# Kernel optimization log

Hardware: AMD Instinct MI355X
Metric: run time of the kernel (lower is better)

Reference implementation:

```python
import jax, jax.numpy as jnp
import numpy as np
import math

B, T, D, H, L = 8, 1024, 128, 8, 2
DH = D // H            # head dim = 16
F = 2 * D              # ffn hidden = 256 (FFN_EXPANSION=2)
SCALE = math.sqrt(DH)  # sqrt of Q last dim per head


def layernorm(x, g, b):
    m = jnp.mean(x, axis=-1, keepdims=True)
    v = jnp.var(x, axis=-1, keepdims=True)
    return (x - m) * jax.lax.rsqrt(v + 1e-5) * g + b


def setup_inputs() -> dict:
    key = jax.random.key(0)
    ks = jax.random.split(key, 16)
    s = 1.0 / math.sqrt(D)
    r = lambda i, shp: jax.random.normal(ks[i], shp, dtype=jnp.float32) * s
    return {
        "x": jax.random.normal(ks[0], (B, T, D), dtype=jnp.float32),
        "y": jax.random.normal(ks[1], (B, T, D), dtype=jnp.float32),
        # shared qkv projections (no bias), per layer
        "Wq": r(2, (L, D, D)), "Wk": r(3, (L, D, D)), "Wv": r(4, (L, D, D)),
        "Wox": r(5, (L, D, D)), "box": jnp.zeros((L, D), jnp.float32),
        "Woy": r(6, (L, D, D)), "boy": jnp.zeros((L, D), jnp.float32),
        "ln1x_g": jnp.ones((L, D), jnp.float32), "ln1x_b": jnp.zeros((L, D), jnp.float32),
        "ln1y_g": jnp.ones((L, D), jnp.float32), "ln1y_b": jnp.zeros((L, D), jnp.float32),
        "ln2x_g": jnp.ones((L, D), jnp.float32), "ln2x_b": jnp.zeros((L, D), jnp.float32),
        "ln2y_g": jnp.ones((L, D), jnp.float32), "ln2y_b": jnp.zeros((L, D), jnp.float32),
        "fx_w1": r(7, (L, D, F)), "fx_b1": jnp.zeros((L, F), jnp.float32),
        "fx_w2": r(8, (L, F, D)), "fx_b2": jnp.zeros((L, D), jnp.float32),
        "fy_w1": r(9, (L, D, F)), "fy_b1": jnp.zeros((L, F), jnp.float32),
        "fy_w2": r(10, (L, F, D)), "fy_b2": jnp.zeros((L, D), jnp.float32),
    }


def _heads(t):
    # (B,T,D) -> (B,T,H,DH)
    return t.reshape(B, T, H, DH)


def _block(x, y, Wq, Wk, Wv, Wox, box, Woy, boy,
           ln1x_g, ln1x_b, ln1y_g, ln1y_b, ln2x_g, ln2x_b, ln2y_g, ln2y_b,
           fx_w1, fx_b1, fx_w2, fx_b2, fy_w1, fy_b1, fy_w2, fy_b2):
    xn = layernorm(x, ln1x_g, ln1x_b)
    yn = layernorm(y, ln1y_g, ln1y_b)
    # x-branch: Q from y, K/V from x ; y-branch: Q from x, K/V from y
    qx = _heads(yn @ Wq); kx = _heads(xn @ Wk); vx = _heads(xn @ Wv)
    qy = _heads(xn @ Wq); ky = _heads(yn @ Wk); vy = _heads(yn @ Wv)
    ax = jnp.einsum('bthd,bshd->bhts', qx, kx)  # (B,H,T,T)
    ay = jnp.einsum('bthd,bshd->bhts', qy, ky)
    # cat over heads + reshape(B,2,H,T,T) + mean(dim=1) == per-head average
    w = jax.nn.softmax((ax + ay) * (0.5 / SCALE), axis=-1)
    o1 = jnp.einsum('bhts,bshd->bthd', w, vx).reshape(B, T, D) @ Wox + box
    o2 = jnp.einsum('bhts,bshd->bthd', w, vy).reshape(B, T, D) @ Woy + boy
    x = x + o1
    y = y + o2
    xn2 = layernorm(x, ln2x_g, ln2x_b)
    yn2 = layernorm(y, ln2y_g, ln2y_b)
    x = x + jax.nn.gelu(xn2 @ fx_w1 + fx_b1, approximate=False) @ fx_w2 + fx_b2
    y = y + jax.nn.gelu(yn2 @ fy_w1 + fy_b1, approximate=False) @ fy_w2 + fy_b2
    return x, y


def reference(x, y, Wq, Wk, Wv, Wox, box, Woy, boy,
              ln1x_g, ln1x_b, ln1y_g, ln1y_b, ln2x_g, ln2x_b, ln2y_g, ln2y_b,
              fx_w1, fx_b1, fx_w2, fx_b2, fy_w1, fy_b1, fy_w2, fy_b2):
    for i in range(L):
        x, y = _block(x, y, Wq[i], Wk[i], Wv[i], Wox[i], box[i], Woy[i], boy[i],
                      ln1x_g[i], ln1x_b[i], ln1y_g[i], ln1y_b[i],
                      ln2x_g[i], ln2x_b[i], ln2y_g[i], ln2y_b[i],
                      fx_w1[i], fx_b1[i], fx_w2[i], fx_b2[i],
                      fy_w1[i], fy_b1[i], fy_w2[i], fy_b2[i])
    return (x, y)
```

## Files before the change

kernel.cpp:

```cpp
#include <hip/hip_runtime.h>
#include <cstddef>

#define BB   8
#define TT   1024
#define DDIM 128
#define HH   8
#define DHH  16
#define FF   256
#define BT   (BB * TT)

typedef unsigned short u16;
typedef __attribute__((ext_vector_type(8))) short short8;
typedef __attribute__((ext_vector_type(4))) float f32x4;

__device__ __forceinline__ u16 bf(float x) {
  unsigned u = __builtin_bit_cast(unsigned, x);
  u += 0x7fffu + ((u >> 16) & 1u);
  return (u16)(u >> 16);
}
__device__ __forceinline__ u16 bft(float x) {
  return (u16)(__builtin_bit_cast(unsigned, x) >> 16);
}
__device__ __forceinline__ float gelu_f(float x) {
  const float t = x * (0.79788456f + 0.03567740814f * x * x);
  return x / (1.0f + __expf(-2.0f * t));
}

__device__ __forceinline__ void qkv_tail(
    const u16* __restrict__ Wq, const u16* __restrict__ Wk, const u16* __restrict__ Wv,
    u16* __restrict__ q_out, u16* __restrict__ k_out, u16* __restrict__ vT_out,
    int m0, u16 (*As)[136], u16 (*Bs)[136]) {
  const int tid = threadIdx.x;
  const int w = tid >> 6, lane = tid & 63, l15 = lane & 15, quad = lane >> 4;
  const int wr = w & 1, wc = w >> 1;
  const u16* Ws[3] = {Wq, Wk, Wv};
  #pragma unroll
  for (int wi = 0; wi < 3; ++wi) {
    #pragma unroll
    for (int t = tid; t < 2048; t += 256) {
      const int r = t >> 4, g8 = (t & 15) << 3;
      *(short8*)&Bs[r][g8] = *(const short8*)(Ws[wi] + (size_t)r * 128 + g8);
    }
    __syncthreads();
    f32x4 acc[4];
    #pragma unroll
    for (int j = 0; j < 4; ++j) acc[j] = {0.f, 0.f, 0.f, 0.f};
    #pragma unroll
    for (int ks = 0; ks < 4; ++ks) {
      const short8 ar = *(const short8*)&As[wr * 16 + l15][ks * 32 + quad * 8];
      #pragma unroll
      for (int j = 0; j < 4; ++j) {
        const short8 br = *(const short8*)&Bs[wc * 64 + j * 16 + l15][ks * 32 + quad * 8];
        acc[j] = __builtin_amdgcn_mfma_f32_16x16x32_bf16(ar, br, acc[j], 0, 0, 0);
      }
    }
    if (wi == 2) {
      const int m_base = m0 + wr * 16 + quad * 4;
      const int bb_ = m_base >> 10, s = m_base & 1023;
      #pragma unroll
      for (int j = 0; j < 4; ++j) {
        const int n = wc * 64 + j * 16 + l15;
        const int h = n >> 4, c = n & 15;
        ushort4 o;
        o.x = bf(acc[j][0]); o.y = bf(acc[j][1]);
        o.z = bf(acc[j][2]); o.w = bf(acc[j][3]);
        *(ushort4*)(vT_out + (((size_t)(bb_ * 8 + h) * 16 + c) << 10) + s) = o;
      }
    } else {
      u16* out = (wi == 0) ? q_out : k_out;
      #pragma unroll
      for (int j = 0; j < 4; ++j) {
        const int n = wc * 64 + j * 16 + l15;
        #pragma unroll
        for (int reg = 0; reg < 4; ++reg) {
          const int m = m0 + wr * 16 + quad * 4 + reg;
          out[(size_t)m * 128 + n] = bf(acc[j][reg]);
        }
      }
    }
    __syncthreads();
  }
}

struct PrepP { const float* W; u16* Wt; int K; int N; };
struct PrepArgs { PrepP p[18]; };

__global__ __launch_bounds__(256) void prep_k(PrepArgs a) {
  const PrepP pp = a.p[blockIdx.z];
  const int n0 = blockIdx.x * 64, k0 = blockIdx.y * 64;
  if (n0 >= pp.N || k0 >= pp.K) return;
  __shared__ float tile[64][65];
  const int tid = threadIdx.x;
  #pragma unroll
  for (int t = tid; t < 1024; t += 256) {
    const int kk = t >> 4, nn4 = (t & 15) << 2;
    float4 v = *(const float4*)(pp.W + (size_t)(k0 + kk) * pp.N + n0 + nn4);
    tile[nn4 + 0][kk] = v.x; tile[nn4 + 1][kk] = v.y;
    tile[nn4 + 2][kk] = v.z; tile[nn4 + 3][kk] = v.w;
  }
  __syncthreads();
  #pragma unroll
  for (int t = tid; t < 1024; t += 256) {
    const int nn = t >> 4, kk4 = (t & 15) << 2;
    ushort4 o;
    o.x = bf(tile[nn][kk4 + 0]); o.y = bf(tile[nn][kk4 + 1]);
    o.z = bf(tile[nn][kk4 + 2]); o.w = bf(tile[nn][kk4 + 3]);
    *(ushort4*)(pp.Wt + (size_t)(n0 + nn) * pp.K + k0 + kk4) = o;
  }
}

struct LnqkvP { const float* in; const float* g; const float* b;
                const u16* Wq; const u16* Wk; const u16* Wv;
                u16* q_out; u16* k_out; u16* vT_out; };
struct LnqkvArgs { LnqkvP p[2]; };

__global__ __launch_bounds__(256) void lnqkv_k(LnqkvArgs a) {
  const LnqkvP pp = a.p[blockIdx.y];
  const int m0 = blockIdx.x * 32;
  __shared__ __align__(16) u16 As[32][136];
  __shared__ __align__(16) u16 Bs[128][136];
  __shared__ float2 stats[32][2];
  const int tid  = threadIdx.x;
  const int w    = tid >> 6;
  const int lane = tid & 63;
  const int l15  = lane & 15;
  const int quad = lane >> 4;
  const int wr = w & 1, wc = w >> 1;

  float xv[4][4];
  #pragma unroll
  for (int j = 0; j < 4; ++j) {
    const int n = wc * 64 + j * 16 + l15;
    #pragma unroll
    for (int reg = 0; reg < 4; ++reg) {
      const int m = m0 + wr * 16 + quad * 4 + reg;
      xv[j][reg] = pp.in[(size_t)m * 128 + n];
    }
  }
  #pragma unroll
  for (int reg = 0; reg < 4; ++reg) {
    float s = 0.f, q = 0.f;
    #pragma unroll
    for (int j = 0; j < 4; ++j) { const float v = xv[j][reg]; s += v; q += v * v; }
    #pragma unroll
    for (int off = 8; off >= 1; off >>= 1) {
      s += __shfl_xor(s, off, 16);
      q += __shfl_xor(q, off, 16);
    }
    if (l15 == 0) stats[wr * 16 + quad * 4 + reg][wc] = make_float2(s, q);
  }
  __syncthreads();
  #pragma unroll
  for (int reg = 0; reg < 4; ++reg) {
    const int mloc = wr * 16 + quad * 4 + reg;
    const float2 s0 = stats[mloc][0], s1 = stats[mloc][1];
    const float mean = (s0.x + s1.x) * (1.0f / 128.f);
    const float var  = (s0.y + s1.y) * (1.0f / 128.f) - mean * mean;
    const float r    = rsqrtf(var + 1e-5f);
    #pragma unroll
    for (int j = 0; j < 4; ++j) {
      const int n = wc * 64 + j * 16 + l15;
      As[mloc][n] = bf((xv[j][reg] - mean) * r * pp.g[n] + pp.b[n]);
    }
  }
  qkv_tail(pp.Wq, pp.Wk, pp.Wv, pp.q_out, pp.k_out, pp.vT_out, m0, As, Bs);
}

struct WofnP { const u16* A; const u16* WoT; const float* bo; const float* res;
               const float* g2; const float* b2l;
               const u16* W1t; const float* b1;
               const u16* W2t; const float* b2;
               float* outF;
               const float* gn; const float* bn;
               const u16* nWq; const u16* nWk; const u16* nWv;
               u16* q_out; u16* k_out; u16* vT_out; };
struct WofnArgs { WofnP p[2]; int ln; };

__global__ __launch_bounds__(256) void wofn_k(WofnArgs a) {
  const WofnP pp = a.p[blockIdx.y];
  const int m0 = blockIdx.x * 32;
  __shared__ __align__(16) u16 As[32][136];
  __shared__ __align__(16) u16 Bs[128][136];
  __shared__ __align__(16) u16 Hs[32][264];
  __shared__ float2 stats[32][2];
  const int tid  = threadIdx.x;
  const int w    = tid >> 6;
  const int lane = tid & 63;
  const int l15  = lane & 15;
  const int quad = lane >> 4;
  const int wr = w & 1, wc = w >> 1;

  #pragma unroll
  for (int t = tid; t < 512; t += 256) {
    const int r = t >> 4, g8 = (t & 15) << 3;
    *(short8*)&As[r][g8] = *(const short8*)(pp.A + (size_t)(m0 + r) * 128 + g8);
  }
  #pragma unroll
  for (int t = tid; t < 2048; t += 256) {
    const int r = t >> 4, g8 = (t & 15) << 3;
    *(short8*)&Bs[r][g8] = *(const short8*)(pp.WoT + (size_t)r * 128 + g8);
  }
  __syncthreads();
  f32x4 acc[4];
  #pragma unroll
  for (int j = 0; j < 4; ++j) acc[j] = {0.f, 0.f, 0.f, 0.f};
  #pragma unroll
  for (int ks = 0; ks < 4; ++ks) {
    const short8 ar = *(const short8*)&As[wr * 16 + l15][ks * 32 + quad * 8];
    #pragma unroll
    for (int j = 0; j < 4; ++j) {
      const short8 br = *(const short8*)&Bs[wc * 64 + j * 16 + l15][ks * 32 + quad * 8];
      acc[j] = __builtin_amdgcn_mfma_f32_16x16x32_bf16(ar, br, acc[j], 0, 0, 0);
    }
  }

  float xv[4][4];
  #pragma unroll
  for (int j = 0; j < 4; ++j) {
    const int n = wc * 64 + j * 16 + l15;
    const float bias_v = pp.bo[n];
    #pragma unroll
    for (int reg = 0; reg < 4; ++reg) {
      const int m = m0 + wr * 16 + quad * 4 + reg;
      xv[j][reg] = acc[j][reg] + bias_v + pp.res[(size_t)m * 128 + n];
    }
  }

  #pragma unroll
  for (int reg = 0; reg < 4; ++reg) {
    float s = 0.f, q = 0.f;
    #pragma unroll
    for (int j = 0; j < 4; ++j) { const float v = xv[j][reg]; s += v; q += v * v; }
    #pragma unroll
    for (int off = 8; off >= 1; off >>= 1) {
      s += __shfl_xor(s, off, 16);
      q += __shfl_xor(q, off, 16);
    }
    if (l15 == 0) stats[wr * 16 + quad * 4 + reg][wc] = make_float2(s, q);
  }
  __syncthreads();
  #pragma unroll
  for (int reg = 0; reg < 4; ++reg) {
    const int mloc = wr * 16 + quad * 4 + reg;
    const float2 s0 = stats[mloc][0], s1 = stats[mloc][1];
    const float mean = (s0.x + s1.x) * (1.0f / 128.f);
    const float var  = (s0.y + s1.y) * (1.0f / 128.f) - mean * mean;
    const float r    = rsqrtf(var + 1e-5f);
    #pragma unroll
    for (int j = 0; j < 4; ++j) {
      const int n = wc * 64 + j * 16 + l15;
      As[mloc][n] = bf((xv[j][reg] - mean) * r * pp.g2[n] + pp.b2l[n]);
    }
  }
  __syncthreads();

  for (int nh = 0; nh < 2; ++nh) {
    #pragma unroll
    for (int t = tid; t < 2048; t += 256) {
      const int r = t >> 4, g8 = (t & 15) << 3;
      *(short8*)&Bs[r][g8] = *(const short8*)(pp.W1t + (size_t)(nh * 128 + r) * 128 + g8);
    }
    __syncthreads();
    f32x4 a1[4];
    #pragma unroll
    for (int j = 0; j < 4; ++j) a1[j] = {0.f, 0.f, 0.f, 0.f};
    #pragma unroll
    for (int ks = 0; ks < 4; ++ks) {
      const short8 ar = *(const short8*)&As[wr * 16 + l15][ks * 32 + quad * 8];
      #pragma unroll
      for (int j = 0; j < 4; ++j) {
        const short8 br = *(const short8*)&Bs[wc * 64 + j * 16 + l15][ks * 32 + quad * 8];
        a1[j] = __builtin_amdgcn_mfma_f32_16x16x32_bf16(ar, br, a1[j], 0, 0, 0);
      }
    }
    #pragma unroll
    for (int j = 0; j < 4; ++j) {
      const int n = wc * 64 + j * 16 + l15;
      const float bias_v = pp.b1[nh * 128 + n];
      #pragma unroll
      for (int reg = 0; reg < 4; ++reg) {
        const int mloc = wr * 16 + quad * 4 + reg;
        Hs[mloc][nh * 128 + n] = bf(gelu_f(a1[j][reg] + bias_v));
      }
    }
    __syncthreads();
  }

  f32x4 a2[4];
  #pragma unroll
  for (int j = 0; j < 4; ++j) a2[j] = {0.f, 0.f, 0.f, 0.f};
  for (int kh = 0; kh < 2; ++kh) {
    #pragma unroll
    for (int t = tid; t < 2048; t += 256) {
      const int r = t >> 4, g8 = (t & 15) << 3;
      *(short8*)&Bs[r][g8] = *(const short8*)(pp.W2t + (size_t)r * 256 + kh * 128 + g8);
    }
    __syncthreads();
    #pragma unroll
    for (int ks = 0; ks < 4; ++ks) {
      const short8 ar = *(const short8*)&Hs[wr * 16 + l15][kh * 128 + ks * 32 + quad * 8];
      #pragma unroll
      for (int j = 0; j < 4; ++j) {
        const short8 br = *(const short8*)&Bs[wc * 64 + j * 16 + l15][ks * 32 + quad * 8];
        a2[j] = __builtin_amdgcn_mfma_f32_16x16x32_bf16(ar, br, a2[j], 0, 0, 0);
      }
    }
    __syncthreads();
  }

  #pragma unroll
  for (int j = 0; j < 4; ++j) {
    const int n = wc * 64 + j * 16 + l15;
    const float bias_v = pp.b2[n];
    #pragma unroll
    for (int reg = 0; reg < 4; ++reg) {
      const int m = m0 + wr * 16 + quad * 4 + reg;
      const float v = a2[j][reg] + bias_v + xv[j][reg];
      xv[j][reg] = v;
      pp.outF[(size_t)m * 128 + n] = v;
    }
  }
  if (!a.ln) return;

  #pragma unroll
  for (int reg = 0; reg < 4; ++reg) {
    float s = 0.f, q = 0.f;
    #pragma unroll
    for (int j = 0; j < 4; ++j) { const float v = xv[j][reg]; s += v; q += v * v; }
    #pragma unroll
    for (int off = 8; off >= 1; off >>= 1) {
      s += __shfl_xor(s, off, 16);
      q += __shfl_xor(q, off, 16);
    }
    if (l15 == 0) stats[wr * 16 + quad * 4 + reg][wc] = make_float2(s, q);
  }
  __syncthreads();
  #pragma unroll
  for (int reg = 0; reg < 4; ++reg) {
    const int mloc = wr * 16 + quad * 4 + reg;
    const float2 s0 = stats[mloc][0], s1 = stats[mloc][1];
    const float mean = (s0.x + s1.x) * (1.0f / 128.f);
    const float var  = (s0.y + s1.y) * (1.0f / 128.f) - mean * mean;
    const float r    = rsqrtf(var + 1e-5f);
    #pragma unroll
    for (int j = 0; j < 4; ++j) {
      const int n = wc * 64 + j * 16 + l15;
      As[mloc][n] = bf((xv[j][reg] - mean) * r * pp.gn[n] + pp.bn[n]);
    }
  }
  qkv_tail(pp.nWq, pp.nWk, pp.nWv, pp.q_out, pp.k_out, pp.vT_out, m0, As, Bs);
}

__global__ __launch_bounds__(256) void attn_k(const u16* __restrict__ qx,
                                              const u16* __restrict__ kx,
                                              const u16* __restrict__ qy,
                                              const u16* __restrict__ ky,
                                              const u16* __restrict__ vtx,
                                              const u16* __restrict__ vty,
                                              u16* __restrict__ o1,
                                              u16* __restrict__ o2) {
  const int t0 = blockIdx.x * 64;
  const int bh = blockIdx.y;
  const int b = bh >> 3, h = bh & 7;
  const size_t base = (size_t)b * TT * DDIM + h * DHH;

  __shared__ __align__(16) u16 Ks[2][64][40];
  __shared__ __align__(16) u16 Vt[2][32][72];
  __shared__ __align__(16) u16 Ps[64][72];

  const int tid  = threadIdx.x;
  const int w    = tid >> 6;
  const int lane = tid & 63;
  const int l15  = lane & 15;
  const int quad = lane >> 4;

  const u16* qp = (quad < 2) ? qx : qy;
  const int dq = (quad & 1) * 8;
  const short8 qa = *(const short8*)(qp + base + (size_t)(t0 + w * 16 + l15) * DDIM + dq);

  f32x4 Of0 = {0.f, 0.f, 0.f, 0.f};
  f32x4 Of1 = {0.f, 0.f, 0.f, 0.f};
  float l_i = 0.f;

  const int ks_s = tid >> 2, ks_c = tid & 3;
  const u16* ks_p = (ks_c < 2) ? kx : ky;
  const int ks_d8 = (ks_c & 1) * 8;
  const int ks_col = (ks_c < 2 ? 0 : 16) + ks_d8;

  const int vs_c = tid >> 3;
  const int vs_s8 = (tid & 7) * 8;
  const u16* vs_row = (vs_c < 16) ? (vtx + (((size_t)bh * 16 + vs_c) << 10))
                                  : (vty + (((size_t)bh * 16 + (vs_c - 16)) << 10));

  #define STAGE(kt, buf)                                                          \
    do {                                                                          \
      const int s0_ = (kt) * 64;                                                  \
      *(short8*)&Ks[buf][ks_s][ks_col] =                                          \
          *(const short8*)(ks_p + base + (size_t)(s0_ + ks_s) * DDIM + ks_d8);    \
      *(short8*)&Vt[buf][vs_c][vs_s8] = *(const short8*)(vs_row + s0_ + vs_s8);   \
    } while (0)

  STAGE(0, 0);

  for (int kt = 0; kt < TT / 64; ++kt) {
    const int buf = kt & 1;
    __syncthreads();
    if (kt + 1 < TT / 64) STAGE(kt + 1, buf ^ 1);

    f32x4 Sf[4];
    #pragma unroll
    for (int t = 0; t < 4; ++t) {
      short8 kb = *(const short8*)&Ks[buf][t * 16 + l15][quad * 8];
      f32x4 z = {0.f, 0.f, 0.f, 0.f};
      Sf[t] = __builtin_amdgcn_mfma_f32_16x16x32_bf16(kb, qa, z, 0, 0, 0);
    }

    #pragma unroll
    for (int t = 0; t < 4; ++t) {
      const float p0 = exp2f(Sf[t][0] * 0.18033688011112042f);
      const float p1 = exp2f(Sf[t][1] * 0.18033688011112042f);
      const float p2 = exp2f(Sf[t][2] * 0.18033688011112042f);
      const float p3 = exp2f(Sf[t][3] * 0.18033688011112042f);
      l_i += p0 + p1 + p2 + p3;
      ushort4 pk;
      pk.x = bft(p0); pk.y = bft(p1); pk.z = bft(p2); pk.w = bft(p3);
      *(ushort4*)&Ps[w * 16 + l15][t * 16 + quad * 4] = pk;
    }

    #pragma unroll
    for (int sh = 0; sh < 2; ++sh) {
      short8 pa  = *(const short8*)&Ps[w * 16 + l15][sh * 32 + quad * 8];
      short8 vb0 = *(const short8*)&Vt[buf][l15][sh * 32 + quad * 8];
      short8 vb1 = *(const short8*)&Vt[buf][16 + l15][sh * 32 + quad * 8];
      Of0 = __builtin_amdgcn_mfma_f32_16x16x32_bf16(pa, vb0, Of0, 0, 0, 0);
      Of1 = __builtin_amdgcn_mfma_f32_16x16x32_bf16(pa, vb1, Of1, 0, 0, 0);
    }
  }
  #undef STAGE

  l_i += __shfl_xor(l_i, 16);
  l_i += __shfl_xor(l_i, 32);
  #pragma unroll
  for (int reg = 0; reg < 4; ++reg) {
    const float lq = __shfl(l_i, quad * 4 + reg, 16);
    const float inv = 1.0f / lq;
    const size_t r = base + (size_t)(t0 + w * 16 + quad * 4 + reg) * DDIM + l15;
    o1[r] = bf(Of0[reg] * inv);
    o2[r] = bf(Of1[reg] * inv);
  }
}

extern "C" void kernel_launch(void* const* d_in, const int* in_sizes, int n_in,
                              void* d_out, int out_size, void* d_ws, size_t ws_size,
                              hipStream_t stream) {
  const float* x_in  = (const float*)d_in[0];
  const float* y_in  = (const float*)d_in[1];
  const float* Wq    = (const float*)d_in[2];
  const float* Wk    = (const float*)d_in[3];
  const float* Wv    = (const float*)d_in[4];
  const float* Wox   = (const float*)d_in[5];
  const float* box   = (const float*)d_in[6];
  const float* Woy   = (const float*)d_in[7];
  const float* boy   = (const float*)d_in[8];
  const float* ln1xg = (const float*)d_in[9];
  const float* ln1xb = (const float*)d_in[10];
  const float* ln1yg = (const float*)d_in[11];
  const float* ln1yb = (const float*)d_in[12];
  const float* ln2xg = (const float*)d_in[13];
  const float* ln2xb = (const float*)d_in[14];
  const float* ln2yg = (const float*)d_in[15];
  const float* ln2yb = (const float*)d_in[16];
  const float* fxw1  = (const float*)d_in[17];
  const float* fxb1  = (const float*)d_in[18];
  const float* fxw2  = (const float*)d_in[19];
  const float* fxb2  = (const float*)d_in[20];
  const float* fyw1  = (const float*)d_in[21];
  const float* fyb1  = (const float*)d_in[22];
  const float* fyw2  = (const float*)d_in[23];
  const float* fyb2  = (const float*)d_in[24];

  const size_t S = (size_t)BT * DDIM;
  float* X = (float*)d_out;
  float* Y = X + S;

  char* wsb = (char*)d_ws;
  auto carve = [&](size_t bytes) { char* p = wsb; wsb += (bytes + 255) & ~(size_t)255; return p; };
  u16* qx  = (u16*)carve(S * 2);
  u16* kx  = (u16*)carve(S * 2);
  u16* qy  = (u16*)carve(S * 2);
  u16* ky  = (u16*)carve(S * 2);
  u16* vxT = (u16*)carve(S * 2);
  u16* vyT = (u16*)carve(S * 2);
  u16* ob1 = (u16*)carve(S * 2);
  u16* ob2 = (u16*)carve(S * 2);
  u16* WqT[2], *WkT[2], *WvT[2], *WoxT[2], *WoyT[2];
  u16* f1xT[2], *f1yT[2], *f2xT[2], *f2yT[2];
  for (int l = 0; l < 2; ++l) {
    WqT[l]  = (u16*)carve(16384 * 2);
    WkT[l]  = (u16*)carve(16384 * 2);
    WvT[l]  = (u16*)carve(16384 * 2);
    WoxT[l] = (u16*)carve(16384 * 2);
    WoyT[l] = (u16*)carve(16384 * 2);
    f1xT[l] = (u16*)carve(32768 * 2);
    f1yT[l] = (u16*)carve(32768 * 2);
    f2xT[l] = (u16*)carve(32768 * 2);
    f2yT[l] = (u16*)carve(32768 * 2);
  }

  {
    PrepArgs a;
    int idx = 0;
    for (int l = 0; l < 2; ++l) {
      a.p[idx++] = {Wq  + (size_t)l * 16384, WqT[l],  128, 128};
      a.p[idx++] = {Wk  + (size_t)l * 16384, WkT[l],  128, 128};
      a.p[idx++] = {Wv  + (size_t)l * 16384, WvT[l],  128, 128};
      a.p[idx++] = {Wox + (size_t)l * 16384, WoxT[l], 128, 128};
      a.p[idx++] = {Woy + (size_t)l * 16384, WoyT[l], 128, 128};
      a.p[idx++] = {fxw1 + (size_t)l * 32768, f1xT[l], 128, 256};
      a.p[idx++] = {fyw1 + (size_t)l * 32768, f1yT[l], 128, 256};
      a.p[idx++] = {fxw2 + (size_t)l * 32768, f2xT[l], 256, 128};
      a.p[idx++] = {fyw2 + (size_t)l * 32768, f2yT[l], 256, 128};
    }
    prep_k<<<dim3(4, 4, 18), 256, 0, stream>>>(a);
  }

  {
    LnqkvArgs a;
    a.p[0] = {x_in, ln1xg, ln1xb, WqT[0], WkT[0], WvT[0], qy, kx, vxT};
    a.p[1] = {y_in, ln1yg, ln1yb, WqT[0], WkT[0], WvT[0], qx, ky, vyT};
    lnqkv_k<<<dim3(BT / 32, 2), 256, 0, stream>>>(a);
  }

  for (int l = 0; l < 2; ++l) {
    const size_t bo  = (size_t)l * DDIM;
    const size_t fbo = (size_t)l * FF;

    attn_k<<<dim3(TT / 64, BB * HH), 256, 0, stream>>>(qx, kx, qy, ky, vxT, vyT, ob1, ob2);

    {
      const float* resx = (l == 0) ? x_in : X;
      const float* resy = (l == 0) ? y_in : Y;
      WofnArgs a = {}; a.ln = (l == 0) ? 1 : 0;
      a.p[0] = {ob1, WoxT[l], box + bo, resx, ln2xg + bo, ln2xb + bo,
                f1xT[l], fxb1 + fbo, f2xT[l], fxb2 + bo, X,
                (l == 0) ? ln1xg + DDIM : nullptr, (l == 0) ? ln1xb + DDIM : nullptr,
                (l == 0) ? WqT[1] : nullptr, (l == 0) ? WkT[1] : nullptr,
                (l == 0) ? WvT[1] : nullptr,
                (l == 0) ? qy : nullptr, (l == 0) ? kx : nullptr,
                (l == 0) ? vxT : nullptr};
      a.p[1] = {ob2, WoyT[l], boy + bo, resy, ln2yg + bo, ln2yb + bo,
                f1yT[l], fyb1 + fbo, f2yT[l], fyb2 + bo, Y,
                (l == 0) ? ln1yg + DDIM : nullptr, (l == 0) ? ln1yb + DDIM : nullptr,
                (l == 0) ? WqT[1] : nullptr, (l == 0) ? WkT[1] : nullptr,
                (l == 0) ? WvT[1] : nullptr,
                (l == 0) ? qx : nullptr, (l == 0) ? ky : nullptr,
                (l == 0) ? vyT : nullptr};
      wofn_k<<<dim3(BT / 32, 2), 256, 0, stream>>>(a);
    }
  }
}
```

Before: 222.0 us.

## Process two query tiles per wave in attention to reuse staged K/V tiles

```diff
diff --git a/kernel.cpp b/kernel.cpp
--- a/kernel.cpp
+++ b/kernel.cpp
@@ -359,14 +359,14 @@
                                               const u16* __restrict__ vty,
                                               u16* __restrict__ o1,
                                               u16* __restrict__ o2) {
-  const int t0 = blockIdx.x * 64;
+  const int t0 = blockIdx.x * 128;
   const int bh = blockIdx.y;
   const int b = bh >> 3, h = bh & 7;
   const size_t base = (size_t)b * TT * DDIM + h * DHH;
 
   __shared__ __align__(16) u16 Ks[2][64][40];
   __shared__ __align__(16) u16 Vt[2][32][72];
-  __shared__ __align__(16) u16 Ps[64][72];
+  __shared__ __align__(16) u16 Ps[128][72];
 
   const int tid  = threadIdx.x;
   const int w    = tid >> 6;
@@ -376,11 +376,15 @@
 
   const u16* qp = (quad < 2) ? qx : qy;
   const int dq = (quad & 1) * 8;
-  const short8 qa = *(const short8*)(qp + base + (size_t)(t0 + w * 16 + l15) * DDIM + dq);
-
-  f32x4 Of0 = {0.f, 0.f, 0.f, 0.f};
-  f32x4 Of1 = {0.f, 0.f, 0.f, 0.f};
-  float l_i = 0.f;
+  short8 qa[2];
+  #pragma unroll
+  for (int u = 0; u < 2; ++u)
+    qa[u] = *(const short8*)(qp + base + (size_t)(t0 + w * 32 + u * 16 + l15) * DDIM + dq);
+
+  f32x4 Of[2][2];
+  #pragma unroll
+  for (int u = 0; u < 2; ++u) { Of[u][0] = {0,0,0,0}; Of[u][1] = {0,0,0,0}; }
+  float l_i[2] = {0.f, 0.f};
 
   const int ks_s = tid >> 2, ks_c = tid & 3;
   const u16* ks_p = (ks_c < 2) ? kx : ky;
@@ -407,46 +411,59 @@
     __syncthreads();
     if (kt + 1 < TT / 64) STAGE(kt + 1, buf ^ 1);
 
-    f32x4 Sf[4];
-    #pragma unroll
-    for (int t = 0; t < 4; ++t) {
-      short8 kb = *(const short8*)&Ks[buf][t * 16 + l15][quad * 8];
-      f32x4 z = {0.f, 0.f, 0.f, 0.f};
-      Sf[t] = __builtin_amdgcn_mfma_f32_16x16x32_bf16(kb, qa, z, 0, 0, 0);
-    }
-
-    #pragma unroll
-    for (int t = 0; t < 4; ++t) {
-      const float p0 = exp2f(Sf[t][0] * 0.18033688011112042f);
-      const float p1 = exp2f(Sf[t][1] * 0.18033688011112042f);
-      const float p2 = exp2f(Sf[t][2] * 0.18033688011112042f);
-      const float p3 = exp2f(Sf[t][3] * 0.18033688011112042f);
-      l_i += p0 + p1 + p2 + p3;
-      ushort4 pk;
-      pk.x = bft(p0); pk.y = bft(p1); pk.z = bft(p2); pk.w = bft(p3);
-      *(ushort4*)&Ps[w * 16 + l15][t * 16 + quad * 4] = pk;
+    short8 kb[4];
+    #pragma unroll
+    for (int t = 0; t < 4; ++t)
+      kb[t] = *(const short8*)&Ks[buf][t * 16 + l15][quad * 8];
+
+    #pragma unroll
+    for (int u = 0; u < 2; ++u) {
+      f32x4 Sf[4];
+      #pragma unroll
+      for (int t = 0; t < 4; ++t) {
+        f32x4 z = {0.f, 0.f, 0.f, 0.f};
+        Sf[t] = __builtin_amdgcn_mfma_f32_16x16x32_bf16(kb[t], qa[u], z, 0, 0, 0);
+      }
+      #pragma unroll
+      for (int t = 0; t < 4; ++t) {
+        const float p0 = exp2f(Sf[t][0] * 0.18033688011112042f);
+        const float p1 = exp2f(Sf[t][1] * 0.18033688011112042f);
+        const float p2 = exp2f(Sf[t][2] * 0.18033688011112042f);
+        const float p3 = exp2f(Sf[t][3] * 0.18033688011112042f);
+        l_i[u] += p0 + p1 + p2 + p3;
+        ushort4 pk;
+        pk.x = bft(p0); pk.y = bft(p1); pk.z = bft(p2); pk.w = bft(p3);
+        *(ushort4*)&Ps[w * 32 + u * 16 + l15][t * 16 + quad * 4] = pk;
+      }
     }
 
     #pragma unroll
     for (int sh = 0; sh < 2; ++sh) {
-      short8 pa  = *(const short8*)&Ps[w * 16 + l15][sh * 32 + quad * 8];
       short8 vb0 = *(const short8*)&Vt[buf][l15][sh * 32 + quad * 8];
       short8 vb1 = *(const short8*)&Vt[buf][16 + l15][sh * 32 + quad * 8];
-      Of0 = __builtin_amdgcn_mfma_f32_16x16x32_bf16(pa, vb0, Of0, 0, 0, 0);
-      Of1 = __builtin_amdgcn_mfma_f32_16x16x32_bf16(pa, vb1, Of1, 0, 0, 0);
+      #pragma unroll
+      for (int u = 0; u < 2; ++u) {
+        short8 pa = *(const short8*)&Ps[w * 32 + u * 16 + l15][sh * 32 + quad * 8];
+        Of[u][0] = __builtin_amdgcn_mfma_f32_16x16x32_bf16(pa, vb0, Of[u][0], 0, 0, 0);
+        Of[u][1] = __builtin_amdgcn_mfma_f32_16x16x32_bf16(pa, vb1, Of[u][1], 0, 0, 0);
+      }
     }
   }
   #undef STAGE
 
-  l_i += __shfl_xor(l_i, 16);
-  l_i += __shfl_xor(l_i, 32);
-  #pragma unroll
-  for (int reg = 0; reg < 4; ++reg) {
-    const float lq = __shfl(l_i, quad * 4 + reg, 16);
-    const float inv = 1.0f / lq;
-    const size_t r = base + (size_t)(t0 + w * 16 + quad * 4 + reg) * DDIM + l15;
-    o1[r] = bf(Of0[reg] * inv);
-    o2[r] = bf(Of1[reg] * inv);
+  #pragma unroll
+  for (int u = 0; u < 2; ++u) {
+    float l = l_i[u];
+    l += __shfl_xor(l, 16);
+    l += __shfl_xor(l, 32);
+    #pragma unroll
+    for (int reg = 0; reg < 4; ++reg) {
+      const float lq = __shfl(l, quad * 4 + reg, 16);
+      const float inv = 1.0f / lq;
+      const size_t r = base + (size_t)(t0 + w * 32 + u * 16 + quad * 4 + reg) * DDIM + l15;
+      o1[r] = bf(Of[u][0][reg] * inv);
+      o2[r] = bf(Of[u][1][reg] * inv);
+    }
   }
 }
 
@@ -535,7 +552,7 @@
     const size_t bo  = (size_t)l * DDIM;
     const size_t fbo = (size_t)l * FF;
 
-    attn_k<<<dim3(TT / 64, BB * HH), 256, 0, stream>>>(qx, kx, qy, ky, vxT, vyT, ob1, ob2);
+    attn_k<<<dim3(TT / 128, BB * HH), 256, 0, stream>>>(qx, kx, qy, ky, vxT, vyT, ob1, ob2);
 
     {
       const float* resx = (l == 0) ? x_in : X;
```

Measured after the change: 226.5 us. +2.1%, slower.
